# Kernel optimization log

Hardware: AMD Instinct MI355X
Metric: run time of the kernel (lower is better)

The kernel has to match this reference:

```python
import jax, jax.numpy as jnp
import numpy as np

EMB = 512
QKV = 512
H = 8      # num_heads
PH = 8     # num_pheads
HD = QKV // H
PHD = QKV // PH


def _make_params(key):
    names = ['Wi', 'Wip', 'Wic', 'Wq', 'Wpq', 'Wk', 'Wpk', 'Wv', 'Wpv', 'Wo', 'Wop']
    ks = jax.random.split(key, len(names))
    p = {}
    for n, k in zip(names, ks):
        din = EMB if n in ('Wi', 'Wip', 'Wic') else QKV
        dout = EMB if n in ('Wo', 'Wop') else QKV
        p[n] = jax.random.normal(k, (din, dout), jnp.float32) * 0.02
        p['b' + n[1:]] = jnp.zeros((dout,), jnp.float32)
    return p


def setup_inputs() -> dict:
    key = jax.random.key(0)
    kq, kp, kc, kw = jax.random.split(key, 4)
    B, S, P = 16, 4096, 64
    inp = {
        'query': jax.random.normal(kq, (B, S, EMB), jnp.float32),
        'pquery': jax.random.normal(kp, (B, P, EMB), jnp.float32),
        'context': jax.random.normal(kc, (B, S, EMB), jnp.float32),
    }
    inp.update(_make_params(kw))
    return inp


def reference(query, pquery, context,
              Wi, bi, Wip, bip, Wic, bic,
              Wq, bq, Wpq, bpq, Wk, bk, Wpk, bpk,
              Wv, bv, Wpv, bpv, Wo, bo, Wop, bop):
    # Dropout layers act as identity (eval mode / deterministic reference).
    B, S, _ = query.shape
    P = pquery.shape[1]

    q_in = query @ Wi + bi        # (B,S,QKV)
    pq_in = pquery @ Wip + bip    # (B,P,QKV)
    c_in = context @ Wic + bic    # (B,S,QKV)

    # --- pack stage: pquery attends over context -> p_context ---
    pq = ((pq_in @ Wpq + bpq) * (PHD ** -0.5)).reshape(B, P, PH, PHD)
    pk = (c_in @ Wpk + bpk).reshape(B, S, PH, PHD)
    pv = (c_in @ Wpv + bpv).reshape(B, S, PH, PHD)
    # dropout before softmax in original; identity here
    pattn = jax.nn.softmax(jnp.einsum('bphd,bshd->bhps', pq, pk), axis=-1)
    pc = jnp.einsum('bhps,bshd->bphd', pattn, pv).reshape(B, P, QKV)

    # --- unpack stage: query attends over p_context ---
    q = ((q_in @ Wq + bq) * (HD ** -0.5)).reshape(B, S, H, HD)
    k = (pc @ Wk + bk).reshape(B, P, H, HD)
    v = (pc @ Wv + bv).reshape(B, P, H, HD)
    aw = jax.nn.softmax(jnp.einsum('bshd,bphd->bhsp', q, k), axis=-1)  # (B,H,S,P)
    attn = jnp.einsum('bhsp,bphd->bshd', aw, v).reshape(B, S, QKV)
    attn = attn @ Wo + bo           # (B,S,EMB)
    pc_out = pc @ Wop + bop         # (B,P,EMB)

    # torch returns attn_weights as (S, B*H, P) when batch_first
    aw_t = jnp.transpose(aw.reshape(B * H, S, P), (1, 0, 2))
    return attn, pc_out, aw_t
```

## Files before the change

### kernel.cpp

```cpp
#include <hip/hip_runtime.h>


typedef __bf16 bf16x8 __attribute__((ext_vector_type(8)));
typedef float f32x4 __attribute__((ext_vector_type(4)));
typedef unsigned short u16x8 __attribute__((ext_vector_type(8)));
typedef unsigned short u16x4 __attribute__((ext_vector_type(4)));

#define MFMA16(a, b, c) __builtin_amdgcn_mfma_f32_16x16x32_bf16((a), (b), (c), 0, 0, 0)

__device__ __forceinline__ unsigned short f2bf_bits(float f) {
  unsigned int u = __float_as_uint(f);
  u += 0x7fffu + ((u >> 16) & 1u);
  return (unsigned short)(u >> 16);
}

__device__ __forceinline__ void gload16(const void* g, void* l) {
  __builtin_amdgcn_global_load_lds(
      (const __attribute__((address_space(1))) void*)g,
      (__attribute__((address_space(3))) void*)l, 16, 0, 0);
}

struct Ptr8 { const float* p[8]; };

__global__ __launch_bounds__(256) void prep_kernel(
    Ptr8 srcs, unsigned short* __restrict__ WT,
    const float* bi, const float* bip, const float* bic,
    const float* Wq, const float* Wpq, const float* Wpk, const float* Wpv,
    const float* bq, const float* bpq, const float* bpk, const float* bpv,
    float* __restrict__ bias_out) {
  const int t = threadIdx.x;
  if (blockIdx.z < 8) {
    const float* __restrict__ W = srcs.p[blockIdx.z];
    unsigned short* __restrict__ O = WT + (size_t)blockIdx.z * 262144;
    __shared__ float tile[32][33];
    const int tr = blockIdx.x * 32, tc = blockIdx.y * 32;
    {
      const int r = t >> 3, c4 = (t & 7) * 4;
      const float4 v = *reinterpret_cast<const float4*>(&W[(size_t)(tr + r) * 512 + tc + c4]);
      tile[r][c4 + 0] = v.x; tile[r][c4 + 1] = v.y; tile[r][c4 + 2] = v.z; tile[r][c4 + 3] = v.w;
    }
    __syncthreads();
    {
      const int n = t >> 3, k4 = (t & 7) * 4;
      u16x4 o;
#pragma unroll
      for (int j = 0; j < 4; j++) o[j] = f2bf_bits(tile[k4 + j][n]);
      *reinterpret_cast<u16x4*>(&O[(size_t)(tc + n) * 512 + tr + k4]) = o;
    }
  } else {
    const int idx = blockIdx.y * 16 + blockIdx.x;
    if (idx >= 8) return;
    const int y = idx >> 1;
    const float* bin  = (y == 0) ? bi : (y == 1) ? bip : bic;
    const float* W    = (y == 0) ? Wq : (y == 1) ? Wpq : (y == 2) ? Wpk : Wpv;
    const float* bout = (y == 0) ? bq : (y == 1) ? bpq : (y == 2) ? bpk : bpv;
    const float scale = (y < 2) ? 0.125f : 1.0f;
    const int n = (idx & 1) * 256 + t;
    float s = 0.f;
    for (int k = 0; k < 512; k++) s += bin[k] * W[(size_t)k * 512 + n];
    bias_out[y * 512 + n] = (s + bout[n]) * scale;
  }
}

__global__ __launch_bounds__(256) void gemm_wcomb(
    const float* __restrict__ Wi, const float* __restrict__ Wip,
    const float* __restrict__ Wic, const unsigned short* __restrict__ WTbase,
    unsigned short* __restrict__ outbase) {
  const int z = blockIdx.z;
  const float* __restrict__ A = (z == 0) ? Wi : (z == 1) ? Wip : Wic;
  const unsigned short* __restrict__ BT = WTbase + (size_t)z * 262144;
  unsigned short* __restrict__ out = outbase + (size_t)z * 262144;
  const float scale = (z < 2) ? 0.125f : 1.0f;

  __shared__ __align__(16) unsigned short As[128 * 72];
  __shared__ __align__(16) unsigned short Bs[128 * 72];
  const int t = threadIdx.x;
  const int w = t >> 6, l = t & 63, li = l & 15, lg = l >> 4;
  const int wm = w >> 1, wn = w & 1;
  const int m0 = blockIdx.x * 128, n0 = blockIdx.y * 128;

  f32x4 acc[4][4] = {};

  for (int kt = 0; kt < 512; kt += 64) {
#pragma unroll
    for (int i = 0; i < 8; i++) {
      const int row = i * 16 + (t >> 4), k = (t & 15) * 4;
      const float4 v = *reinterpret_cast<const float4*>(&A[(size_t)(m0 + row) * 512 + kt + k]);
      u16x4 o;
      o[0] = f2bf_bits(v.x); o[1] = f2bf_bits(v.y);
      o[2] = f2bf_bits(v.z); o[3] = f2bf_bits(v.w);
      *reinterpret_cast<u16x4*>(&As[row * 72 + k]) = o;
    }
#pragma unroll
    for (int i = 0; i < 4; i++) {
      const int row = i * 32 + (t >> 3), k = (t & 7) * 8;
      const u16x8 v = *reinterpret_cast<const u16x8*>(&BT[(size_t)(n0 + row) * 512 + kt + k]);
      *reinterpret_cast<u16x8*>(&Bs[row * 72 + k]) = v;
    }
    __syncthreads();
#pragma unroll
    for (int kk = 0; kk < 2; kk++) {
      bf16x8 a[4], b[4];
#pragma unroll
      for (int mf = 0; mf < 4; mf++)
        a[mf] = *reinterpret_cast<const bf16x8*>(&As[(wm * 64 + mf * 16 + li) * 72 + kk * 32 + lg * 8]);
#pragma unroll
      for (int nf = 0; nf < 4; nf++)
        b[nf] = *reinterpret_cast<const bf16x8*>(&Bs[(wn * 64 + nf * 16 + li) * 72 + kk * 32 + lg * 8]);
#pragma unroll
      for (int mf = 0; mf < 4; mf++)
#pragma unroll
        for (int nf = 0; nf < 4; nf++)
          acc[mf][nf] = MFMA16(a[mf], b[nf], acc[mf][nf]);
    }
    __syncthreads();
  }
  const int lg4 = lg * 4;
#pragma unroll
  for (int nf = 0; nf < 4; nf++) {
    const int col = n0 + wn * 64 + nf * 16 + li;
#pragma unroll
    for (int mf = 0; mf < 4; mf++) {
      const int row = m0 + wm * 64 + mf * 16 + lg4;
#pragma unroll
      for (int r = 0; r < 4; r++)
        out[(size_t)col * 512 + row + r] = f2bf_bits(acc[mf][nf][r] * scale);
    }
  }
}

#define WAITV(n)                                            \
  {                                                         \
    asm volatile("s_waitcnt vmcnt(" #n ")" ::: "memory");   \
    __builtin_amdgcn_sched_barrier(0);                      \
  }
#define WAITLGKM()                                          \
  {                                                         \
    asm volatile("s_waitcnt lgkmcnt(0)" ::: "memory");      \
    __builtin_amdgcn_sched_barrier(0);                      \
  }
#define BAR3()                                              \
  {                                                         \
    __builtin_amdgcn_s_barrier();                           \
    __builtin_amdgcn_sched_barrier(0);                      \
  }

__device__ __forceinline__ void gemm_hyb_body(
    const float* __restrict__ A, const unsigned short* __restrict__ BT,
    const float* __restrict__ bias, unsigned short* __restrict__ out,
    int Ntiles, int ldc, int wg) {
  __shared__ __align__(16) unsigned short As[2][128 * 32];
  __shared__ __align__(16) unsigned short Bs[3][128 * 32];
  const int t = threadIdx.x;
  const int w = t >> 6, l = t & 63, li = l & 15, lg = l >> 4;
  const int wm = w >> 1, wn = w & 1;
  const int m0 = (wg / Ntiles) * 128, n0 = (wg % Ntiles) * 128;

  f32x4 acc[4][4] = {};
  float4 ra[2][2];
  const int rrow = t >> 2;
  const int slot = (t & 3) ^ ((t >> 3) & 3);
  const float* aptr = A + (size_t)(m0 + rrow) * 512 + slot * 8;

#define ISSUE_A(kt)                                                            \
  {                                                                            \
    ra[0][0] = *reinterpret_cast<const float4*>(aptr + (kt));                  \
    ra[0][1] = *reinterpret_cast<const float4*>(aptr + (kt) + 4);              \
    ra[1][0] = *reinterpret_cast<const float4*>(aptr + 64 * 512 + (kt));       \
    ra[1][1] = *reinterpret_cast<const float4*>(aptr + 64 * 512 + (kt) + 4);   \
  }

#define CVT_WRITE_A(buf)                                                       \
  {                                                                            \
    _Pragma("unroll") for (int i = 0; i < 2; i++) {                            \
      bf16x8 v;                                                                \
      _Pragma("unroll") for (int j = 0; j < 4; j++) {                          \
        v[j] = (__bf16)ra[i][0][j];                                            \
        v[j + 4] = (__bf16)ra[i][1][j];                                        \
      }                                                                        \
      *reinterpret_cast<bf16x8*>(&As[buf][(i * 256 + t) * 8]) = v;             \
    }                                                                          \
  }

#define STAGE_B(tile)                                                          \
  {                                                                            \
    const int bb = (tile) % 3;                                                 \
    const int kt = (tile) * 32;                                                \
    _Pragma("unroll") for (int i = 0; i < 2; i++) {                            \
      const int row = i * 64 + rrow;                                           \
      gload16(&BT[(size_t)(n0 + row) * 512 + kt + slot * 8],                   \
              &Bs[bb][(i * 256 + t) * 8]);                                     \
    }                                                                          \
  }

#define COMPUTE(tile)                                                          \
  {                                                                            \
    const int ab = (tile) & 1;                                                 \
    const int bb = (tile) % 3;                                                 \
    bf16x8 a[4], b[4];                                                         \
    _Pragma("unroll") for (int mf = 0; mf < 4; mf++) {                         \
      const int r = wm * 64 + mf * 16 + li;                                    \
      a[mf] = *reinterpret_cast<const bf16x8*>(                                \
          &As[ab][r * 32 + ((lg ^ ((r >> 1) & 3)) * 8)]);                      \
    }                                                                          \
    _Pragma("unroll") for (int nf = 0; nf < 4; nf++) {                         \
      const int r = wn * 64 + nf * 16 + li;                                    \
      b[nf] = *reinterpret_cast<const bf16x8*>(                                \
          &Bs[bb][r * 32 + ((lg ^ ((r >> 1) & 3)) * 8)]);                      \
    }                                                                          \
    _Pragma("unroll") for (int mf = 0; mf < 4; mf++)                           \
        _Pragma("unroll") for (int nf = 0; nf < 4; nf++)                       \
            acc[mf][nf] = MFMA16(a[mf], b[nf], acc[mf][nf]);                   \
  }

  ISSUE_A(0);
  STAGE_B(0);
  STAGE_B(1);
  WAITV(4);
  CVT_WRITE_A(0);
  ISSUE_A(32);

#pragma unroll 1
  for (int tt = 0; tt < 15; ++tt) {
    WAITV(2);
    CVT_WRITE_A((tt + 1) & 1);
    if (tt < 14) {
      ISSUE_A((tt + 2) * 32);
      STAGE_B(tt + 2);
    }
    WAITLGKM();
    BAR3();
    COMPUTE(tt);
    BAR3();
  }
  WAITV(0);
  BAR3();
  COMPUTE(15);

#undef ISSUE_A
#undef CVT_WRITE_A
#undef STAGE_B
#undef COMPUTE

  const int lg4 = lg * 4;
#pragma unroll
  for (int nf = 0; nf < 4; nf++) {
    const int col = n0 + wn * 64 + nf * 16 + li;
    const float bv = bias[col];
#pragma unroll
    for (int mf = 0; mf < 4; mf++) {
      const int row = m0 + wm * 64 + mf * 16 + lg4;
#pragma unroll
      for (int r = 0; r < 4; r++)
        out[(size_t)(row + r) * ldc + col] = f2bf_bits(acc[mf][nf][r] + bv);
    }
  }
}

__global__ __launch_bounds__(256, 4) void gemm_hyb_qpkv(
    const float* query, const float* context, const float* pquery,
    const unsigned short* WqeT, const unsigned short* WpkveT,
    const unsigned short* WpqeT, const float* bqe, const float* bpkve,
    const float* bpqe, unsigned short* q_buf, unsigned short* pkv_buf,
    unsigned short* pq_buf) {
  const int q8 = gridDim.x >> 3;
  int wg = ((int)blockIdx.x & 7) * q8 + ((int)blockIdx.x >> 3);
  const float* A;
  const unsigned short* BT;
  const float* bias;
  unsigned short* out;
  int Ntiles, ldc;
  if (wg < 2048) {
    A = query; BT = WqeT; bias = bqe; out = q_buf; Ntiles = 4; ldc = 512;
  } else if (wg < 6144) {
    wg -= 2048; A = context; BT = WpkveT; bias = bpkve; out = pkv_buf;
    Ntiles = 8; ldc = 1024;
  } else {
    wg -= 6144; A = pquery; BT = WpqeT; bias = bpqe; out = pq_buf;
    Ntiles = 4; ldc = 512;
  }
  gemm_hyb_body(A, BT, bias, out, Ntiles, ldc, wg);
}

__device__ __forceinline__ void gemm3p_body_f32out(
    const unsigned short* __restrict__ A, const unsigned short* __restrict__ BT,
    const float* __restrict__ bias, float* __restrict__ out, int Ntiles,
    int ldc, int wg) {
  __shared__ __align__(16) unsigned short As[3][128 * 32];
  __shared__ __align__(16) unsigned short Bs[3][128 * 32];
  const int t = threadIdx.x;
  const int w = t >> 6, l = t & 63, li = l & 15, lg = l >> 4;
  const int wm = w >> 1, wn = w & 1;
  const int m0 = (wg / Ntiles) * 128, n0 = (wg % Ntiles) * 128;

  f32x4 acc[4][4] = {};
  const int srow = t >> 2, sslot = t & 3;

#define STAGE3(tile)                                                           \
  {                                                                            \
    const int bb = (tile) % 3;                                                 \
    const int kt = (tile) * 32;                                                \
    _Pragma("unroll") for (int i = 0; i < 2; i++) {                            \
      const int row = i * 64 + srow;                                           \
      const int gs = (sslot ^ ((row >> 1) & 3)) * 8;                           \
      gload16(&A[(size_t)(m0 + row) * 512 + kt + gs], &As[bb][(i * 256 + t) * 8]); \
    }                                                                          \
    _Pragma("unroll") for (int i = 0; i < 2; i++) {                            \
      const int row = i * 64 + srow;                                           \
      const int gs = (sslot ^ ((row >> 1) & 3)) * 8;                           \
      gload16(&BT[(size_t)(n0 + row) * 512 + kt + gs], &Bs[bb][(i * 256 + t) * 8]); \
    }                                                                          \
  }

#define COMPUTE3(tile)                                                         \
  {                                                                            \
    const int bb = (tile) % 3;                                                 \
    bf16x8 a[4], b[4];                                                         \
    _Pragma("unroll") for (int mf = 0; mf < 4; mf++) {                         \
      const int r = wm * 64 + mf * 16 + li;                                    \
      a[mf] = *reinterpret_cast<const bf16x8*>(                                \
          &As[bb][r * 32 + ((lg ^ ((r >> 1) & 3)) * 8)]);                      \
    }                                                                          \
    _Pragma("unroll") for (int nf = 0; nf < 4; nf++) {                         \
      const int r = wn * 64 + nf * 16 + li;                                    \
      b[nf] = *reinterpret_cast<const bf16x8*>(                                \
          &Bs[bb][r * 32 + ((lg ^ ((r >> 1) & 3)) * 8)]);                      \
    }                                                                          \
    _Pragma("unroll") for (int mf = 0; mf < 4; mf++)                           \
        _Pragma("unroll") for (int nf = 0; nf < 4; nf++)                       \
            acc[mf][nf] = MFMA16(a[mf], b[nf], acc[mf][nf]);                   \
  }

  STAGE3(0);
  STAGE3(1);
  STAGE3(2);

#pragma unroll 1
  for (int tt = 0; tt < 13; ++tt) {
    WAITV(8);
    BAR3();
    COMPUTE3(tt);
    BAR3();
    STAGE3(tt + 3);
  }
  WAITV(8); BAR3(); COMPUTE3(13); BAR3();
  WAITV(4); BAR3(); COMPUTE3(14); BAR3();
  WAITV(0); BAR3(); COMPUTE3(15);

#undef STAGE3
#undef COMPUTE3

  const int lg4 = lg * 4;
#pragma unroll
  for (int nf = 0; nf < 4; nf++) {
    const int col = n0 + wn * 64 + nf * 16 + li;
    const float bv = bias[col];
#pragma unroll
    for (int mf = 0; mf < 4; mf++) {
      const int row = m0 + wm * 64 + mf * 16 + lg4;
#pragma unroll
      for (int r = 0; r < 4; r++)
        out[(size_t)(row + r) * ldc + col] = acc[mf][nf][r] + bv;
    }
  }
}

__global__ __launch_bounds__(256, 3) void gemm3p_final(
    const unsigned short* A, const unsigned short* BT, const float* bias,
    float* out) {
  const int q8 = gridDim.x >> 3;
  const int wg = ((int)blockIdx.x & 7) * q8 + ((int)blockIdx.x >> 3);
  gemm3p_body_f32out(A, BT, bias, out, 4, 512, wg);
}

__global__ __launch_bounds__(256) void gemm_kvpc(
    const unsigned short* __restrict__ A, const unsigned short* __restrict__ BT,
    const float* __restrict__ bias0, const float* __restrict__ bias1,
    const float* __restrict__ bias2, unsigned short* out0, unsigned short* out1,
    float* out2, int Ntiles) {
  __shared__ __align__(16) unsigned short As[128 * 64];
  __shared__ __align__(16) unsigned short Bs[128 * 64];
  const int t = threadIdx.x;
  const int w = t >> 6, l = t & 63, li = l & 15, lg = l >> 4;
  const int wm = w >> 1, wn = w & 1;
  const int K = 512;
  const int m0 = (blockIdx.x / Ntiles) * 128, n0 = (blockIdx.x % Ntiles) * 128;

  f32x4 acc[4][4] = {};
  const int sr = t >> 3, sslot = t & 7;

  for (int kt = 0; kt < K; kt += 64) {
#pragma unroll
    for (int i = 0; i < 4; i++) {
      const int row = i * 32 + sr;
      const int gs = (sslot ^ (row & 7)) * 8;
      gload16(&A[(size_t)(m0 + row) * K + kt + gs], &As[(i * 256 + t) * 8]);
      gload16(&BT[(size_t)(n0 + row) * K + kt + gs], &Bs[(i * 256 + t) * 8]);
    }
    __syncthreads();
#pragma unroll
    for (int kk = 0; kk < 2; kk++) {
      bf16x8 a[4], b[4];
#pragma unroll
      for (int mf = 0; mf < 4; mf++) {
        const int r = wm * 64 + mf * 16 + li;
        a[mf] = *reinterpret_cast<const bf16x8*>(&As[r * 64 + (((kk * 4 + lg) ^ (r & 7)) * 8)]);
      }
#pragma unroll
      for (int nf = 0; nf < 4; nf++) {
        const int r = wn * 64 + nf * 16 + li;
        b[nf] = *reinterpret_cast<const bf16x8*>(&Bs[r * 64 + (((kk * 4 + lg) ^ (r & 7)) * 8)]);
      }
#pragma unroll
      for (int mf = 0; mf < 4; mf++)
#pragma unroll
        for (int nf = 0; nf < 4; nf++)
          acc[mf][nf] = MFMA16(a[mf], b[nf], acc[mf][nf]);
    }
    __syncthreads();
  }

  const int lg4 = lg * 4;
#pragma unroll
  for (int nf = 0; nf < 4; nf++) {
    const int col = n0 + wn * 64 + nf * 16 + li;
    if (col < 512) {
      const float bv = bias0[col];
#pragma unroll
      for (int mf = 0; mf < 4; mf++) {
        const int row = m0 + wm * 64 + mf * 16 + lg4;
#pragma unroll
        for (int r = 0; r < 4; r++)
          out0[(size_t)(row + r) * 512 + col] = f2bf_bits(acc[mf][nf][r] + bv);
      }
    } else if (col < 1024) {
      const float bv = bias1[col - 512];
#pragma unroll
      for (int mf = 0; mf < 4; mf++) {
        const int row = m0 + wm * 64 + mf * 16 + lg4;
#pragma unroll
        for (int r = 0; r < 4; r++)
          out1[(size_t)(row + r) * 512 + col - 512] = f2bf_bits(acc[mf][nf][r] + bv);
      }
    } else {
      const float bv = bias2[col - 1024];
#pragma unroll
      for (int mf = 0; mf < 4; mf++) {
        const int row = m0 + wm * 64 + mf * 16 + lg4;
#pragma unroll
        for (int r = 0; r < 4; r++)
          out2[(size_t)(row + r) * 512 + col - 1024] = acc[mf][nf][r] + bv;
      }
    }
  }
}

__global__ __launch_bounds__(256) void pack_attn(
    const unsigned short* __restrict__ pq_buf,
    const unsigned short* __restrict__ pkv_buf, float* __restrict__ partial) {
  __shared__ __align__(16) unsigned short pkL[64 * 72];
  __shared__ __align__(16) unsigned short pvT[64 * 72];
  __shared__ __align__(16) unsigned short prL[4 * 16 * 72];
  const int t = threadIdx.x, w = t >> 6, l = t & 63, li = l & 15, lg = l >> 4;
  const int bh = blockIdx.x, b = bh >> 3, h = bh & 7;
  const int sb = blockIdx.y * 512;

  bf16x8 aq[2];
  {
    const size_t base = ((size_t)(b * 64 + w * 16 + li)) * 512 + h * 64;
    aq[0] = *reinterpret_cast<const bf16x8*>(&pq_buf[base + lg * 8]);
    aq[1] = *reinterpret_cast<const bf16x8*>(&pq_buf[base + 32 + lg * 8]);
  }

  f32x4 acc[4] = {};
  float lsum[4] = {};

  for (int st = 0; st < 8; st++) {
    const int s0 = sb + st * 64;
#pragma unroll
    for (int i = 0; i < 2; i++) {
      const int row = i * 32 + (t >> 3), c = (t & 7) * 8;
      const u16x8 v = *reinterpret_cast<const u16x8*>(
          &pkv_buf[((size_t)(b * 4096 + s0 + row)) * 1024 + h * 64 + c]);
      *reinterpret_cast<u16x8*>(&pkL[row * 72 + c]) = v;
    }
    {
      const int rp = t >> 3, c = (t & 7) * 8;
      const size_t base = ((size_t)(b * 4096 + s0 + 2 * rp)) * 1024 + 512 + h * 64 + c;
      const u16x8 u0 = *reinterpret_cast<const u16x8*>(&pkv_buf[base]);
      const u16x8 u1 = *reinterpret_cast<const u16x8*>(&pkv_buf[base + 1024]);
#pragma unroll
      for (int j = 0; j < 8; j++) {
        const int val = ((int)u0[j] & 0xffff) | ((int)u1[j] << 16);
        *reinterpret_cast<int*>(&pvT[(c + j) * 72 + 2 * rp]) = val;
      }
    }
    __syncthreads();
    f32x4 sc[4] = {};
#pragma unroll
    for (int nf = 0; nf < 4; nf++) {
#pragma unroll
      for (int kk = 0; kk < 2; kk++) {
        const bf16x8 bk = *reinterpret_cast<const bf16x8*>(
            &pkL[(nf * 16 + li) * 72 + kk * 32 + lg * 8]);
        sc[nf] = MFMA16(aq[kk], bk, sc[nf]);
      }
    }
#pragma unroll
    for (int nf = 0; nf < 4; nf++) {
#pragma unroll
      for (int r = 0; r < 4; r++) {
        const float e = __expf(sc[nf][r]);
        lsum[r] += e;
        prL[(w * 16 + lg * 4 + r) * 72 + nf * 16 + li] = f2bf_bits(e);
      }
    }
#pragma unroll
    for (int kk = 0; kk < 2; kk++) {
      const bf16x8 ap = *reinterpret_cast<const bf16x8*>(
          &prL[(w * 16 + li) * 72 + kk * 32 + lg * 8]);
#pragma unroll
      for (int nf = 0; nf < 4; nf++) {
        const bf16x8 bv = *reinterpret_cast<const bf16x8*>(
            &pvT[(nf * 16 + li) * 72 + kk * 32 + lg * 8]);
        acc[nf] = MFMA16(ap, bv, acc[nf]);
      }
    }
    __syncthreads();
  }

#pragma unroll
  for (int m = 1; m < 16; m <<= 1)
#pragma unroll
    for (int r = 0; r < 4; r++) lsum[r] += __shfl_xor(lsum[r], m);

  const size_t pbase = ((size_t)(bh * 8 + blockIdx.y)) * 4160;
#pragma unroll
  for (int nf = 0; nf < 4; nf++)
#pragma unroll
    for (int r = 0; r < 4; r++)
      partial[pbase + (size_t)(w * 16 + lg * 4 + r) * 64 + nf * 16 + li] = acc[nf][r];
  if (li == 0)
#pragma unroll
    for (int r = 0; r < 4; r++) partial[pbase + 4096 + w * 16 + lg * 4 + r] = lsum[r];
}

__global__ __launch_bounds__(256) void pack_combine(const float* __restrict__ partial,
                                                    unsigned short* __restrict__ pc_buf) {
  const int bh = blockIdx.x, b = bh >> 3, h = bh & 7;
  const int t = threadIdx.x;
#pragma unroll
  for (int e = 0; e < 16; e++) {
    const int idx = e * 256 + t;
    const int p = idx >> 6, d = idx & 63;
    float s = 0.f, den = 0.f;
#pragma unroll
    for (int c = 0; c < 8; c++) {
      const float* pb = &partial[((size_t)(bh * 8 + c)) * 4160];
      s += pb[idx];
      den += pb[4096 + p];
    }
    pc_buf[((size_t)(b * 64 + p)) * 512 + h * 64 + d] = f2bf_bits(s / den);
  }
}

__global__ __launch_bounds__(256) void unpack_attn(
    const unsigned short* q_in, const unsigned short* __restrict__ k_buf,
    const unsigned short* __restrict__ v_buf, float* __restrict__ aw_out,
    unsigned short* attnh_out) {
  __shared__ __align__(16) unsigned short kL[64 * 72];
  __shared__ __align__(16) unsigned short vT[64 * 72];
  __shared__ __align__(16) unsigned short prL[4 * 64 * 72];
  const int t = threadIdx.x, w = t >> 6, l = t & 63, li = l & 15, lg = l >> 4;
  const int bh = blockIdx.y, b = bh >> 3, h = bh & 7;
  const int sbase = blockIdx.x * 256 + w * 64;

#pragma unroll
  for (int i = 0; i < 2; i++) {
    const int p = i * 32 + (t >> 3), c = (t & 7) * 8;
    const u16x8 v = *reinterpret_cast<const u16x8*>(
        &k_buf[((size_t)(b * 64 + p)) * 512 + h * 64 + c]);
    *reinterpret_cast<u16x8*>(&kL[p * 72 + c]) = v;
  }
  {
    const int rp = t >> 3, c = (t & 7) * 8;
    const size_t base = ((size_t)(b * 64 + 2 * rp)) * 512 + h * 64 + c;
    const u16x8 u0 = *reinterpret_cast<const u16x8*>(&v_buf[base]);
    const u16x8 u1 = *reinterpret_cast<const u16x8*>(&v_buf[base + 512]);
#pragma unroll
    for (int j = 0; j < 8; j++) {
      const int val = ((int)u0[j] & 0xffff) | ((int)u1[j] << 16);
      *reinterpret_cast<int*>(&vT[(c + j) * 72 + 2 * rp]) = val;
    }
  }
  bf16x8 aq[4][2];
#pragma unroll
  for (int mf = 0; mf < 4; mf++) {
    const size_t base = ((size_t)(b * 4096 + sbase + mf * 16 + li)) * 512 + h * 64;
    aq[mf][0] = *reinterpret_cast<const bf16x8*>(&q_in[base + lg * 8]);
    aq[mf][1] = *reinterpret_cast<const bf16x8*>(&q_in[base + 32 + lg * 8]);
  }
  __syncthreads();

  f32x4 sc[4][4] = {};
#pragma unroll
  for (int kk = 0; kk < 2; kk++)
#pragma unroll
    for (int nf = 0; nf < 4; nf++) {
      const bf16x8 bk = *reinterpret_cast<const bf16x8*>(
          &kL[(nf * 16 + li) * 72 + kk * 32 + lg * 8]);
#pragma unroll
      for (int mf = 0; mf < 4; mf++) sc[mf][nf] = MFMA16(aq[mf][kk], bk, sc[mf][nf]);
    }

#pragma unroll
  for (int mf = 0; mf < 4; mf++) {
#pragma unroll
    for (int r = 0; r < 4; r++) {
      float e[4];
      float rs = 0.f;
#pragma unroll
      for (int nf = 0; nf < 4; nf++) {
        e[nf] = __expf(sc[mf][nf][r]);
        rs += e[nf];
      }
#pragma unroll
      for (int m = 1; m < 16; m <<= 1) rs += __shfl_xor(rs, m);
      const float inv = 1.0f / rs;
      const int srow = sbase + mf * 16 + lg * 4 + r;
#pragma unroll
      for (int nf = 0; nf < 4; nf++) {
        const float pr = e[nf] * inv;
        aw_out[(size_t)srow * 8192 + bh * 64 + nf * 16 + li] = pr;
        prL[(w * 64 + mf * 16 + lg * 4 + r) * 72 + nf * 16 + li] = f2bf_bits(pr);
      }
    }
  }

  f32x4 acc[4][4] = {};
#pragma unroll
  for (int kk = 0; kk < 2; kk++)
#pragma unroll
    for (int mf = 0; mf < 4; mf++) {
      const bf16x8 ap = *reinterpret_cast<const bf16x8*>(
          &prL[(w * 64 + mf * 16 + li) * 72 + kk * 32 + lg * 8]);
#pragma unroll
      for (int nf = 0; nf < 4; nf++) {
        const bf16x8 bv = *reinterpret_cast<const bf16x8*>(
            &vT[(nf * 16 + li) * 72 + kk * 32 + lg * 8]);
        acc[mf][nf] = MFMA16(ap, bv, acc[mf][nf]);
      }
    }
#pragma unroll
  for (int mf = 0; mf < 4; mf++)
#pragma unroll
    for (int nf = 0; nf < 4; nf++)
#pragma unroll
      for (int r = 0; r < 4; r++)
        attnh_out[((size_t)(b * 4096 + sbase + mf * 16 + lg * 4 + r)) * 512 + h * 64 +
                  nf * 16 + li] = f2bf_bits(acc[mf][nf][r]);
}

extern "C" void kernel_launch(void* const* d_in, const int* in_sizes, int n_in,
                              void* d_out, int out_size, void* d_ws, size_t ws_size,
                              hipStream_t stream) {
  (void)in_sizes; (void)n_in; (void)out_size; (void)ws_size;

  const float* query   = (const float*)d_in[0];
  const float* pquery  = (const float*)d_in[1];
  const float* context = (const float*)d_in[2];
  const float* Wi  = (const float*)d_in[3];  const float* bi  = (const float*)d_in[4];
  const float* Wip = (const float*)d_in[5];  const float* bip = (const float*)d_in[6];
  const float* Wic = (const float*)d_in[7];  const float* bic = (const float*)d_in[8];
  const float* Wq  = (const float*)d_in[9];  const float* bq  = (const float*)d_in[10];
  const float* Wpq = (const float*)d_in[11]; const float* bpq = (const float*)d_in[12];
  const float* Wk  = (const float*)d_in[13]; const float* bk  = (const float*)d_in[14];
  const float* Wpk = (const float*)d_in[15]; const float* bpk = (const float*)d_in[16];
  const float* Wv  = (const float*)d_in[17]; const float* bv  = (const float*)d_in[18];
  const float* Wpv = (const float*)d_in[19]; const float* bpv = (const float*)d_in[20];
  const float* Wo  = (const float*)d_in[21]; const float* bo  = (const float*)d_in[22];
  const float* Wop = (const float*)d_in[23]; const float* bop = (const float*)d_in[24];

  char* ws = (char*)d_ws;
  unsigned short* WT     = (unsigned short*)(ws);
  unsigned short* WqeT   = (unsigned short*)(ws + 4u * 1024 * 1024);
  unsigned short* WpqeT  = WqeT + 512 * 512;
  unsigned short* WpkveT = WpqeT + 512 * 512;
  float* bqe   = (float*)(WpkveT + (size_t)1024 * 512);
  float* bpqe  = bqe + 512;
  float* bpkve = bpqe + 512;
  unsigned short* q_buf   = (unsigned short*)(ws + 8u * 1024 * 1024);
  unsigned short* pkv_buf = q_buf + (size_t)65536 * 512;
  unsigned short* pq_buf  = pkv_buf + (size_t)65536 * 1024;
  unsigned short* pc_buf  = pq_buf + (size_t)1024 * 512;
  unsigned short* k_buf   = pc_buf + (size_t)1024 * 512;
  unsigned short* v_buf   = k_buf + (size_t)1024 * 512;
  float* partial = (float*)(v_buf + (size_t)1024 * 512);

  float* out_attn = (float*)d_out;
  float* out_pc   = out_attn + (size_t)16 * 4096 * 512;
  float* out_aw   = out_pc + (size_t)16 * 64 * 512;

  const dim3 blk(256);

  Ptr8 tsrc; tsrc.p[0]=Wq; tsrc.p[1]=Wpq; tsrc.p[2]=Wpk; tsrc.p[3]=Wpv;
  tsrc.p[4]=Wk; tsrc.p[5]=Wv; tsrc.p[6]=Wop; tsrc.p[7]=Wo;
  prep_kernel<<<dim3(16, 16, 9), blk, 0, stream>>>(
      tsrc, WT, bi, bip, bic, Wq, Wpq, Wpk, Wpv, bq, bpq, bpk, bpv, bqe);
  gemm_wcomb<<<dim3(4, 4, 4), blk, 0, stream>>>(Wi, Wip, Wic, WT, WqeT);

  gemm_hyb_qpkv<<<dim3(6176), blk, 0, stream>>>(
      query, context, pquery, WqeT, WpkveT, WpqeT, bqe, bpkve, bpqe,
      q_buf, pkv_buf, pq_buf);

  pack_attn<<<dim3(128, 8), blk, 0, stream>>>(pq_buf, pkv_buf, partial);
  pack_combine<<<128, blk, 0, stream>>>(partial, pc_buf);

  gemm_kvpc<<<dim3(96), blk, 0, stream>>>(
      pc_buf, WT + (size_t)4 * 262144, bk, bv, bop, k_buf, v_buf, out_pc, 12);

  unpack_attn<<<dim3(16, 128), blk, 0, stream>>>(q_buf, k_buf, v_buf, out_aw, q_buf);

  gemm3p_final<<<dim3(2048), blk, 0, stream>>>(
      q_buf, WT + (size_t)7 * 262144, bo, out_attn);
}
```

Measured before the change: 507.3 us.

## Deepen A-operand register prefetch to three stages and fully unroll GEMM loop

```diff
diff --git a/kernel.cpp b/kernel.cpp
--- a/kernel.cpp
+++ b/kernel.cpp
@@ -157,26 +157,26 @@
   const int m0 = (wg / Ntiles) * 128, n0 = (wg % Ntiles) * 128;
 
   f32x4 acc[4][4] = {};
-  float4 ra[2][2];
+  float4 ra0[2][2], ra1[2][2], ra2[2][2];
   const int rrow = t >> 2;
   const int slot = (t & 3) ^ ((t >> 3) & 3);
   const float* aptr = A + (size_t)(m0 + rrow) * 512 + slot * 8;
 
-#define ISSUE_A(kt)                                                            \
+#define ISSUE_A(kt, R)                                                         \
   {                                                                            \
-    ra[0][0] = *reinterpret_cast<const float4*>(aptr + (kt));                  \
-    ra[0][1] = *reinterpret_cast<const float4*>(aptr + (kt) + 4);              \
-    ra[1][0] = *reinterpret_cast<const float4*>(aptr + 64 * 512 + (kt));       \
-    ra[1][1] = *reinterpret_cast<const float4*>(aptr + 64 * 512 + (kt) + 4);   \
-  }
-
-#define CVT_WRITE_A(buf)                                                       \
+    R[0][0] = *reinterpret_cast<const float4*>(aptr + (kt));                   \
+    R[0][1] = *reinterpret_cast<const float4*>(aptr + (kt) + 4);               \
+    R[1][0] = *reinterpret_cast<const float4*>(aptr + 64 * 512 + (kt));        \
+    R[1][1] = *reinterpret_cast<const float4*>(aptr + 64 * 512 + (kt) + 4);    \
+  }
+
+#define CVT_WRITE_A(buf, R)                                                    \
   {                                                                            \
     _Pragma("unroll") for (int i = 0; i < 2; i++) {                            \
       bf16x8 v;                                                                \
       _Pragma("unroll") for (int j = 0; j < 4; j++) {                          \
-        v[j] = (__bf16)ra[i][0][j];                                            \
-        v[j + 4] = (__bf16)ra[i][1][j];                                        \
+        v[j] = (__bf16)R[i][0][j];                                             \
+        v[j + 4] = (__bf16)R[i][1][j];                                         \
       }                                                                        \
       *reinterpret_cast<bf16x8*>(&As[buf][(i * 256 + t) * 8]) = v;             \
     }                                                                          \
@@ -213,26 +213,53 @@
             acc[mf][nf] = MFMA16(a[mf], b[nf], acc[mf][nf]);                   \
   }
 
-  ISSUE_A(0);
+#define GBODY(TT, CV, IS)                                                      \
+  WAITV(6);                                                                    \
+  CVT_WRITE_A(((TT) + 1) & 1, CV);                                             \
+  ISSUE_A(((TT) + 3) * 32, IS);                                                \
+  STAGE_B((TT) + 2);                                                           \
+  WAITLGKM();                                                                  \
+  BAR3();                                                                      \
+  COMPUTE(TT);                                                                 \
+  BAR3();
+
+  ISSUE_A(0, ra0);
   STAGE_B(0);
+  ISSUE_A(32, ra1);
   STAGE_B(1);
-  WAITV(4);
-  CVT_WRITE_A(0);
-  ISSUE_A(32);
-
-#pragma unroll 1
-  for (int tt = 0; tt < 15; ++tt) {
-    WAITV(2);
-    CVT_WRITE_A((tt + 1) & 1);
-    if (tt < 14) {
-      ISSUE_A((tt + 2) * 32);
-      STAGE_B(tt + 2);
-    }
-    WAITLGKM();
-    BAR3();
-    COMPUTE(tt);
-    BAR3();
-  }
+  WAITV(6);
+  CVT_WRITE_A(0, ra0);
+  ISSUE_A(64, ra2);
+  WAITLGKM();
+  BAR3();
+
+  GBODY(0, ra1, ra0)
+  GBODY(1, ra2, ra1)
+  GBODY(2, ra0, ra2)
+  GBODY(3, ra1, ra0)
+  GBODY(4, ra2, ra1)
+  GBODY(5, ra0, ra2)
+  GBODY(6, ra1, ra0)
+  GBODY(7, ra2, ra1)
+  GBODY(8, ra0, ra2)
+  GBODY(9, ra1, ra0)
+  GBODY(10, ra2, ra1)
+  GBODY(11, ra0, ra2)
+  GBODY(12, ra1, ra0)
+
+  WAITV(6);
+  CVT_WRITE_A(0, ra2);
+  STAGE_B(15);
+  WAITLGKM();
+  BAR3();
+  COMPUTE(13);
+  BAR3();
+  WAITV(2);
+  CVT_WRITE_A(1, ra0);
+  WAITLGKM();
+  BAR3();
+  COMPUTE(14);
+  BAR3();
   WAITV(0);
   BAR3();
   COMPUTE(15);
@@ -241,6 +268,7 @@
 #undef CVT_WRITE_A
 #undef STAGE_B
 #undef COMPUTE
+#undef GBODY
 
   const int lg4 = lg * 4;
 #pragma unroll
```

New measurement: 541.8 us. 6.8% more time.

## Widen hybrid input-projection GEMM tiles to 128x256 with 512-thread blocks

Applied to the files above, without the earlier changes.

```diff
diff --git a/kernel.cpp b/kernel.cpp
--- a/kernel.cpp
+++ b/kernel.cpp
@@ -145,41 +145,36 @@
     __builtin_amdgcn_sched_barrier(0);                      \
   }
 
-__device__ __forceinline__ void gemm_hyb_body(
+__device__ __forceinline__ void gemm_hyb512_body(
     const float* __restrict__ A, const unsigned short* __restrict__ BT,
     const float* __restrict__ bias, unsigned short* __restrict__ out,
-    int Ntiles, int ldc, int wg) {
+    int m0, int n0, int ldc) {
   __shared__ __align__(16) unsigned short As[2][128 * 32];
-  __shared__ __align__(16) unsigned short Bs[3][128 * 32];
+  __shared__ __align__(16) unsigned short Bs[3][256 * 32];
   const int t = threadIdx.x;
   const int w = t >> 6, l = t & 63, li = l & 15, lg = l >> 4;
-  const int wm = w >> 1, wn = w & 1;
-  const int m0 = (wg / Ntiles) * 128, n0 = (wg % Ntiles) * 128;
+  const int wm = w >> 2, wn = w & 3;
 
   f32x4 acc[4][4] = {};
-  float4 ra[2][2];
+  float4 ra[2];
   const int rrow = t >> 2;
   const int slot = (t & 3) ^ ((t >> 3) & 3);
   const float* aptr = A + (size_t)(m0 + rrow) * 512 + slot * 8;
 
 #define ISSUE_A(kt)                                                            \
   {                                                                            \
-    ra[0][0] = *reinterpret_cast<const float4*>(aptr + (kt));                  \
-    ra[0][1] = *reinterpret_cast<const float4*>(aptr + (kt) + 4);              \
-    ra[1][0] = *reinterpret_cast<const float4*>(aptr + 64 * 512 + (kt));       \
-    ra[1][1] = *reinterpret_cast<const float4*>(aptr + 64 * 512 + (kt) + 4);   \
+    ra[0] = *reinterpret_cast<const float4*>(aptr + (kt));                     \
+    ra[1] = *reinterpret_cast<const float4*>(aptr + (kt) + 4);                 \
   }
 
 #define CVT_WRITE_A(buf)                                                       \
   {                                                                            \
-    _Pragma("unroll") for (int i = 0; i < 2; i++) {                            \
-      bf16x8 v;                                                                \
-      _Pragma("unroll") for (int j = 0; j < 4; j++) {                          \
-        v[j] = (__bf16)ra[i][0][j];                                            \
-        v[j + 4] = (__bf16)ra[i][1][j];                                        \
-      }                                                                        \
-      *reinterpret_cast<bf16x8*>(&As[buf][(i * 256 + t) * 8]) = v;             \
+    bf16x8 v;                                                                  \
+    _Pragma("unroll") for (int j = 0; j < 4; j++) {                            \
+      v[j] = (__bf16)ra[0][j];                                                 \
+      v[j + 4] = (__bf16)ra[1][j];                                             \
     }                                                                          \
+    *reinterpret_cast<bf16x8*>(&As[buf][t * 8]) = v;                           \
   }
 
 #define STAGE_B(tile)                                                          \
@@ -187,9 +182,9 @@
     const int bb = (tile) % 3;                                                 \
     const int kt = (tile) * 32;                                                \
     _Pragma("unroll") for (int i = 0; i < 2; i++) {                            \
-      const int row = i * 64 + rrow;                                           \
+      const int row = i * 128 + rrow;                                          \
       gload16(&BT[(size_t)(n0 + row) * 512 + kt + slot * 8],                   \
-              &Bs[bb][(i * 256 + t) * 8]);                                     \
+              &Bs[bb][(i * 512 + t) * 8]);                                     \
     }                                                                          \
   }
 
@@ -257,7 +252,7 @@
   }
 }
 
-__global__ __launch_bounds__(256, 4) void gemm_hyb_qpkv(
+__global__ __launch_bounds__(512, 4) void gemm_hyb_qpkv(
     const float* query, const float* context, const float* pquery,
     const unsigned short* WqeT, const unsigned short* WpkveT,
     const unsigned short* WpqeT, const float* bqe, const float* bpkve,
@@ -265,21 +260,18 @@
     unsigned short* pq_buf) {
   const int q8 = gridDim.x >> 3;
   int wg = ((int)blockIdx.x & 7) * q8 + ((int)blockIdx.x >> 3);
-  const float* A;
-  const unsigned short* BT;
-  const float* bias;
-  unsigned short* out;
-  int Ntiles, ldc;
-  if (wg < 2048) {
-    A = query; BT = WqeT; bias = bqe; out = q_buf; Ntiles = 4; ldc = 512;
-  } else if (wg < 6144) {
-    wg -= 2048; A = context; BT = WpkveT; bias = bpkve; out = pkv_buf;
-    Ntiles = 8; ldc = 1024;
+  if (wg < 1024) {
+    gemm_hyb512_body(query, WqeT, bqe, q_buf,
+                     (wg >> 1) * 128, (wg & 1) * 256, 512);
+  } else if (wg < 3072) {
+    wg -= 1024;
+    gemm_hyb512_body(context, WpkveT, bpkve, pkv_buf,
+                     (wg >> 2) * 128, (wg & 3) * 256, 1024);
   } else {
-    wg -= 6144; A = pquery; BT = WpqeT; bias = bpqe; out = pq_buf;
-    Ntiles = 4; ldc = 512;
-  }
-  gemm_hyb_body(A, BT, bias, out, Ntiles, ldc, wg);
+    wg -= 3072;
+    gemm_hyb512_body(pquery, WpqeT, bpqe, pq_buf,
+                     (wg >> 1) * 128, (wg & 1) * 256, 512);
+  }
 }
 
 __device__ __forceinline__ void gemm3p_body_f32out(
@@ -709,7 +701,7 @@
       tsrc, WT, bi, bip, bic, Wq, Wpq, Wpk, Wpv, bq, bpq, bpk, bpv, bqe);
   gemm_wcomb<<<dim3(4, 4, 4), blk, 0, stream>>>(Wi, Wip, Wic, WT, WqeT);
 
-  gemm_hyb_qpkv<<<dim3(6176), blk, 0, stream>>>(
+  gemm_hyb_qpkv<<<dim3(3088), dim3(512), 0, stream>>>(
       query, context, pquery, WqeT, WpkveT, WpqeT, bqe, bpkve, bpqe,
       q_buf, pkv_buf, pq_buf);
 
```

New measurement: 514.5 us. About the same (+1.4%).
